# Kernel tuning notes

Hardware: AMD Instinct MI355X
Metric: run time of the kernel (lower is better)

The kernel has to match this reference:

```python
import jax, jax.numpy as jnp
import numpy as np

N = 100000      # nodes
E = 3200000     # directed edges (before self loops)
F_IN = 512      # input node features
HID = 16        # hidden dim (hardcoded in module)
C = 32          # num_classes
NEG_SLOPE = 0.2 # PyG GATConv default


def setup_inputs() -> dict:
    key = jax.random.key(0)
    ks = jax.random.split(key, 10)
    x = jax.random.normal(ks[0], (N, F_IN), dtype=jnp.float32)
    edge_index = jax.random.randint(ks[1], (2, E), 0, N, dtype=jnp.int64)
    s1 = 1.0 / np.sqrt(F_IN)
    s2 = 1.0 / np.sqrt(HID)
    return {
        "x": x,
        "edge_index": edge_index,
        "W1": jax.random.normal(ks[2], (F_IN, HID), dtype=jnp.float32) * s1,
        "att_src1": jax.random.normal(ks[3], (HID,), dtype=jnp.float32) * s2,
        "att_dst1": jax.random.normal(ks[4], (HID,), dtype=jnp.float32) * s2,
        "b1": jnp.zeros((HID,), dtype=jnp.float32),
        "W2": jax.random.normal(ks[5], (HID, C), dtype=jnp.float32) * s2,
        "att_src2": jax.random.normal(ks[6], (C,), dtype=jnp.float32) / np.sqrt(C),
        "att_dst2": jax.random.normal(ks[7], (C,), dtype=jnp.float32) / np.sqrt(C),
        "b2": jnp.zeros((C,), dtype=jnp.float32),
    }


def gat_conv(h_in, src, dst, W, att_src, att_dst, b, n):
    # h: [n, d_out] transformed node features (lin has no bias in PyG GATConv)
    h = h_in @ W
    a_s = h @ att_src        # [n] per-node source score
    a_d = h @ att_dst        # [n] per-node dest score
    e = jax.nn.leaky_relu(a_s[src] + a_d[dst], NEG_SLOPE)  # [n_edges]
    # segment softmax over edges grouped by destination node
    m = jax.ops.segment_max(e, dst, num_segments=n)
    ex = jnp.exp(e - m[dst])
    denom = jax.ops.segment_sum(ex, dst, num_segments=n)
    alpha = ex / denom[dst]
    out = jax.ops.segment_sum(h[src] * alpha[:, None], dst, num_segments=n)
    return out + b


def reference(x, edge_index, W1, att_src1, att_dst1, b1, W2, att_src2, att_dst2, b2):
    n = x.shape[0]
    loops = jnp.arange(n, dtype=edge_index.dtype)  # add_self_loops=True
    src = jnp.concatenate([edge_index[0], loops])
    dst = jnp.concatenate([edge_index[1], loops])
    h = gat_conv(x, src, dst, W1, att_src1, att_dst1, b1, n)
    h = jax.nn.relu(h)
    # dropout is identity in eval mode
    out = gat_conv(h, src, dst, W2, att_src2, att_dst2, b2, n)
    return jax.nn.log_softmax(out, axis=1)
```

## Files before the change

### kernel.cpp

```cpp
#include <hip/hip_runtime.h>
#include <math.h>

#define N_NODES 100000
#define N_EDGES 3200000
#define N_TOT   (N_EDGES + N_NODES)
#define F_IN    512
#define HID     16
#define NCLS    32
#define NEG_SLOPE 0.2f

#define BSH   7
#define NBKT  ((N_NODES + 127) / 128)
#define SRC_MASK 0x1FFFF

#define G_GROUPS 512
#define EPG (N_EDGES / G_GROUPS)
#define NGEMM ((N_NODES + 127) / 128)

__global__ __launch_bounds__(64) void k_detect(const int* __restrict__ ei,
                                               int* __restrict__ flag) {
  int v = ei[2 * threadIdx.x + 1];
  unsigned long long m = __ballot(v != 0);
  if (threadIdx.x == 0) *flag = (m == 0ull) ? 1 : 0;
}

__global__ __launch_bounds__(512) void k_g1h(const float* __restrict__ x,
                                             const float* __restrict__ W,
                                             const float* __restrict__ atts,
                                             const float* __restrict__ attd,
                                             const int* __restrict__ ei,
                                             const int* __restrict__ flag,
                                             int* __restrict__ H,
                                             const float* __restrict__ W2,
                                             const float* __restrict__ as2w,
                                             const float* __restrict__ ad2w,
                                             float* __restrict__ ws2,
                                             float* __restrict__ wd2,
                                             float* __restrict__ h,
                                             float* __restrict__ as_,
                                             float* __restrict__ ad_) {
  __shared__ float smem[2 * 128 * 36];
  int bid = blockIdx.x;
  int t = threadIdx.x;

  if (bid >= NGEMM) {
    if (bid < NGEMM + G_GROUPS) {
      int* hh = (int*)smem;
      for (int i = t; i < NBKT; i += 512) hh[i] = 0;
      __syncthreads();
      int fl = *flag;
      int g = bid - NGEMM;
      int e0 = g * EPG, e1 = e0 + EPG;
      for (int e = e0 + t; e < e1; e += 512) {
        int d = fl ? ei[2 * (N_EDGES + e)] : ei[N_EDGES + e];
        d = min(max(d, 0), N_NODES - 1);
        atomicAdd(&hh[d >> BSH], 1);
      }
      __syncthreads();
      int* Hrow = H + (size_t)g * NBKT;
      for (int i = t; i < NBKT; i += 512) Hrow[i] = hh[i];
    } else {
      if (t < HID) {
        float s = 0.f, d = 0.f;
        for (int c = 0; c < NCLS; ++c) {
          float wv = W2[t * NCLS + c];
          s += wv * as2w[c];
          d += wv * ad2w[c];
        }
        ws2[t] = s;
        wd2[t] = d;
      }
    }
    return;
  }

  float (*xs)[128][36] = (float (*)[128][36])smem;
  float* pacc = smem;
  int wid = t >> 6;
  int lane = t & 63;
  int rhalf = wid & 1;
  int kq = __builtin_amdgcn_readfirstlane(wid >> 1);
  int row = rhalf * 64 + lane;
  int r0 = bid * 128;

  int sr = t >> 3;
  int sk4 = t & 7;
  int sr2 = (t + 512) >> 3;
  int sk42 = (t + 512) & 7;
  int gr1 = min(r0 + sr, N_NODES - 1);
  int gr2 = min(r0 + sr2, N_NODES - 1);

  float acc[HID];
#pragma unroll
  for (int f = 0; f < HID; ++f) acc[f] = 0.f;

  float4 ra, rb;
  ra = *(const float4*)(x + (size_t)gr1 * F_IN + sk4 * 4);
  rb = *(const float4*)(x + (size_t)gr2 * F_IN + sk42 * 4);
  *(float4*)(&xs[0][sr][sk4 * 4]) = ra;
  *(float4*)(&xs[0][sr2][sk42 * 4]) = rb;
  __syncthreads();

  for (int c = 0; c < F_IN / 32; ++c) {
    int buf = c & 1;
    if (c + 1 < F_IN / 32) {
      ra = *(const float4*)(x + (size_t)gr1 * F_IN + (c + 1) * 32 + sk4 * 4);
      rb = *(const float4*)(x + (size_t)gr2 * F_IN + (c + 1) * 32 + sk42 * 4);
    }
    const float* Wc = W + (c * 32 + kq * 8) * HID;
    float4 xa = *(const float4*)(&xs[buf][row][kq * 8 + 0]);
    float4 xb = *(const float4*)(&xs[buf][row][kq * 8 + 4]);
#pragma unroll
    for (int f = 0; f < HID; ++f)
      acc[f] += xa.x * Wc[0 * HID + f] + xa.y * Wc[1 * HID + f] +
                xa.z * Wc[2 * HID + f] + xa.w * Wc[3 * HID + f];
#pragma unroll
    for (int f = 0; f < HID; ++f)
      acc[f] += xb.x * Wc[4 * HID + f] + xb.y * Wc[5 * HID + f] +
                xb.z * Wc[6 * HID + f] + xb.w * Wc[7 * HID + f];
    if (c + 1 < F_IN / 32) {
      *(float4*)(&xs[buf ^ 1][sr][sk4 * 4]) = ra;
      *(float4*)(&xs[buf ^ 1][sr2][sk42 * 4]) = rb;
    }
    __syncthreads();
  }

#pragma unroll
  for (int f = 0; f < HID; ++f) pacc[(kq * 128 + row) * 17 + f] = acc[f];
  __syncthreads();

  int rr = t >> 2, g = t & 3;
  float4 s;
  s.x = pacc[(0 * 128 + rr) * 17 + g * 4 + 0] + pacc[(1 * 128 + rr) * 17 + g * 4 + 0] +
        pacc[(2 * 128 + rr) * 17 + g * 4 + 0] + pacc[(3 * 128 + rr) * 17 + g * 4 + 0];
  s.y = pacc[(0 * 128 + rr) * 17 + g * 4 + 1] + pacc[(1 * 128 + rr) * 17 + g * 4 + 1] +
        pacc[(2 * 128 + rr) * 17 + g * 4 + 1] + pacc[(3 * 128 + rr) * 17 + g * 4 + 1];
  s.z = pacc[(0 * 128 + rr) * 17 + g * 4 + 2] + pacc[(1 * 128 + rr) * 17 + g * 4 + 2] +
        pacc[(2 * 128 + rr) * 17 + g * 4 + 2] + pacc[(3 * 128 + rr) * 17 + g * 4 + 2];
  s.w = pacc[(0 * 128 + rr) * 17 + g * 4 + 3] + pacc[(1 * 128 + rr) * 17 + g * 4 + 3] +
        pacc[(2 * 128 + rr) * 17 + g * 4 + 3] + pacc[(3 * 128 + rr) * 17 + g * 4 + 3];
  int orow = r0 + rr;
  if (orow < N_NODES) ((float4*)(h + (size_t)orow * HID))[g] = s;

  float4 av = ((const float4*)atts)[g];
  float4 dv = ((const float4*)attd)[g];
  float pas = s.x * av.x + s.y * av.y + s.z * av.z + s.w * av.w;
  float pad = s.x * dv.x + s.y * dv.y + s.z * dv.z + s.w * dv.w;
  pas += __shfl_xor(pas, 1); pas += __shfl_xor(pas, 2);
  pad += __shfl_xor(pad, 1); pad += __shfl_xor(pad, 2);
  if (g == 0 && orow < N_NODES) { as_[orow] = pas; ad_[orow] = pad; }
}

__global__ __launch_bounds__(G_GROUPS) void k_colscan(int* __restrict__ H,
                                                      int* __restrict__ tot) {
  __shared__ int s[G_GROUPS];
  int b = blockIdx.x, t = threadIdx.x;
  int v = H[(size_t)t * NBKT + b];
  s[t] = v;
  __syncthreads();
  for (int off = 1; off < G_GROUPS; off <<= 1) {
    int a = (t >= off) ? s[t - off] : 0;
    __syncthreads();
    s[t] += a;
    __syncthreads();
  }
  H[(size_t)t * NBKT + b] = s[t] - v;
  if (t == G_GROUPS - 1) tot[b] = s[t];
}

__global__ __launch_bounds__(256) void k_bscan(const int* __restrict__ tot,
                                               int* __restrict__ bbase,
                                               int* __restrict__ cbase,
                                               int* __restrict__ offs) {
  __shared__ int s1[256], s2[256];
  int t = threadIdx.x;
  int c[4], vn[4];
  int sum1 = 0, sum2 = 0;
#pragma unroll
  for (int j = 0; j < 4; ++j) {
    int idx = t * 4 + j;
    int cc = 0, vv = 0;
    if (idx < NBKT) {
      cc = tot[idx];
      int lo = idx << BSH;
      vv = min(128, N_NODES - lo);
    }
    c[j] = cc; vn[j] = vv;
    sum1 += cc; sum2 += cc + vv;
  }
  int o1 = sum1, o2 = sum2;
  s1[t] = sum1; s2[t] = sum2;
  __syncthreads();
  for (int off = 1; off < 256; off <<= 1) {
    int a = 0, b = 0;
    if (t >= off) { a = s1[t - off]; b = s2[t - off]; }
    __syncthreads();
    s1[t] += a; s2[t] += b;
    __syncthreads();
  }
  int r1 = s1[t] - o1;
  int r2 = s2[t] - o2;
#pragma unroll
  for (int j = 0; j < 4; ++j) {
    int idx = t * 4 + j;
    if (idx < NBKT) {
      bbase[idx] = r1; cbase[idx] = r2;
      r1 += c[j];
      r2 += c[j] + vn[j];
    }
  }
  if (t == 0) offs[N_NODES] = N_TOT;
}

__global__ __launch_bounds__(256) void k_scatter(const int* __restrict__ ei,
                                                 const int* __restrict__ flag,
                                                 const int* __restrict__ H,
                                                 const int* __restrict__ bbase,
                                                 int* __restrict__ binned) {
  __shared__ int cur[NBKT];
  int g = blockIdx.x, t = threadIdx.x;
  const int* Hrow = H + (size_t)g * NBKT;
  for (int i = t; i < NBKT; i += 256) cur[i] = bbase[i] + Hrow[i];
  __syncthreads();
  int fl = *flag;
  int e0 = g * EPG, e1 = e0 + EPG;
  for (int e = e0 + t; e < e1; e += 256) {
    int s, d;
    if (fl) { s = ei[2 * e]; d = ei[2 * (N_EDGES + e)]; }
    else    { s = ei[e];     d = ei[N_EDGES + e]; }
    s = min(max(s, 0), N_NODES - 1);
    d = min(max(d, 0), N_NODES - 1);
    int p = atomicAdd(&cur[d >> BSH], 1);
    p = min(max(p, 0), N_EDGES - 1);
    binned[p] = ((d & 127) << 17) | s;
  }
}

__global__ __launch_bounds__(256) void k_bucket(const int* __restrict__ tot,
                                                const int* __restrict__ bbase,
                                                const int* __restrict__ cbase,
                                                const int* __restrict__ binned,
                                                int* __restrict__ offs,
                                                int* __restrict__ srcS) {
  __shared__ int cnt[128], cur[128], sc[128];
  __shared__ int hdr[3];
  int b = blockIdx.x, t = threadIdx.x;
  if (t == 0) {
    hdr[0] = min(max(tot[b], 0), N_EDGES);
    hdr[1] = min(max(bbase[b], 0), N_EDGES - 1);
    hdr[2] = min(max(cbase[b], 0), N_TOT - 1);
  }
  if (t < 128) cnt[t] = 0;
  __syncthreads();
  int nb = hdr[0], base = hdr[1], cb = hdr[2];

  for (int i = t; i < nb; i += 256) {
    int pk = binned[min(base + i, N_EDGES - 1)];
    atomicAdd(&cnt[(pk >> 17) & 127], 1);
  }
  __syncthreads();

  int node = (b << BSH) + t;
  int myv = 0;
  if (t < 128) myv = (node < N_NODES) ? cnt[t] + 1 : 0;
  if (t < 128) sc[t] = myv;
  __syncthreads();
  for (int off = 1; off < 128; off <<= 1) {
    int v = 0;
    if (t < 128 && t >= off) v = sc[t - off];
    __syncthreads();
    if (t < 128) sc[t] += v;
    __syncthreads();
  }
  if (t < 128 && node < N_NODES) {
    int lofs = sc[t] - myv;
    int o = min(cb + lofs, N_TOT - 1);
    offs[node] = o;
    srcS[o] = node;
    cur[t] = lofs + 1;
  }
  __syncthreads();

  for (int i = t; i < nb; i += 256) {
    int pk = binned[min(base + i, N_EDGES - 1)];
    int p = atomicAdd(&cur[(pk >> 17) & 127], 1);
    srcS[min(cb + p, N_TOT - 1)] = pk & SRC_MASK;
  }
}

template <bool LAYER1>
__global__ __launch_bounds__(256) void k_agg(const int* __restrict__ offs,
                                             const int* __restrict__ srcS,
                                             const float* __restrict__ as_,
                                             const float* __restrict__ ad_,
                                             const float* __restrict__ h,
                                             const float* __restrict__ b1,
                                             const float* __restrict__ ws2,
                                             const float* __restrict__ wd2,
                                             const float* __restrict__ W2,
                                             const float* __restrict__ b2,
                                             float* __restrict__ outv,
                                             float* __restrict__ as2,
                                             float* __restrict__ ad2) {
  int node = blockIdx.x * 4 + (threadIdx.x >> 6);
  if (node >= N_NODES) return;
  int lane = threadIdx.x & 63;
  int esub = lane >> 2;
  int f4 = lane & 3;
  int beg = offs[node];
  int end = offs[node + 1];
  beg = min(max(beg, 0), N_TOT);
  end = min(max(end, beg), N_TOT);
  float ad = ad_[node];

  float s_lane = 0.f;
  float4 acc = make_float4(0.f, 0.f, 0.f, 0.f);
  for (int i0 = beg; i0 < end; i0 += 64) {
    int nb = min(64, end - i0);
    int sn = 0;
    float p = 0.f;
    if (lane < nb) {
      sn = min(max(srcS[i0 + lane], 0), N_NODES - 1);
      float e = as_[sn] + ad;
      e = e > 0.f ? e : NEG_SLOPE * e;
      p = __expf(e);
    }
    s_lane += p;
    int steps = (nb + 15) >> 4;
    for (int t = 0; t < steps; ++t) {
      int j = esub + 16 * t;
      int jj = min(j, nb - 1);
      float pj = __shfl(p, jj);
      int snj = __shfl(sn, jj);
      if (j < nb) {
        float4 v = ((const float4*)(h + (size_t)snj * HID))[f4];
        acc.x += pj * v.x;
        acc.y += pj * v.y;
        acc.z += pj * v.z;
        acc.w += pj * v.w;
      }
    }
  }
#pragma unroll
  for (int off = 1; off < 64; off <<= 1) s_lane += __shfl_xor(s_lane, off);
#pragma unroll
  for (int off = 4; off < 64; off <<= 1) {
    acc.x += __shfl_xor(acc.x, off);
    acc.y += __shfl_xor(acc.y, off);
    acc.z += __shfl_xor(acc.z, off);
    acc.w += __shfl_xor(acc.w, off);
  }
  float inv_s = 1.f / s_lane;

  if (LAYER1) {
    float4 bv = ((const float4*)b1)[f4];
    float4 val;
    val.x = fmaxf(acc.x * inv_s + bv.x, 0.f);
    val.y = fmaxf(acc.y * inv_s + bv.y, 0.f);
    val.z = fmaxf(acc.z * inv_s + bv.z, 0.f);
    val.w = fmaxf(acc.w * inv_s + bv.w, 0.f);
    if (lane < 4) ((float4*)(outv + (size_t)node * HID))[lane] = val;
    float4 w_s = ((const float4*)ws2)[f4];
    float4 w_d = ((const float4*)wd2)[f4];
    float rs = val.x * w_s.x + val.y * w_s.y + val.z * w_s.z + val.w * w_s.w;
    float rd = val.x * w_d.x + val.y * w_d.y + val.z * w_d.z + val.w * w_d.w;
    rs += __shfl_xor(rs, 1); rs += __shfl_xor(rs, 2);
    rd += __shfl_xor(rd, 1); rd += __shfl_xor(rd, 2);
    if (lane == 0) { as2[node] = rs; ad2[node] = rd; }
  } else {
    float hv[HID];
#pragma unroll
    for (int j = 0; j < 4; ++j) {
      int srcl = (lane & ~3) | j;
      hv[4 * j + 0] = __shfl(acc.x, srcl) * inv_s;
      hv[4 * j + 1] = __shfl(acc.y, srcl) * inv_s;
      hv[4 * j + 2] = __shfl(acc.z, srcl) * inv_s;
      hv[4 * j + 3] = __shfl(acc.w, srcl) * inv_s;
    }
    int c = lane & 31;
    float logit = b2[c];
#pragma unroll
    for (int k = 0; k < HID; ++k) logit += hv[k] * W2[k * NCLS + c];
    float mx = logit;
#pragma unroll
    for (int off = 1; off < 32; off <<= 1) mx = fmaxf(mx, __shfl_xor(mx, off));
    float ex = __expf(logit - mx);
    float se = ex;
#pragma unroll
    for (int off = 1; off < 32; off <<= 1) se += __shfl_xor(se, off);
    if (lane < 32) outv[(size_t)node * NCLS + c] = logit - mx - __logf(se);
  }
}

extern "C" void kernel_launch(void* const* d_in, const int* in_sizes, int n_in,
                              void* d_out, int out_size, void* d_ws, size_t ws_size,
                              hipStream_t stream) {
  const float* x    = (const float*)d_in[0];
  const int*   ei   = (const int*)d_in[1];
  const float* W1   = (const float*)d_in[2];
  const float* as1w = (const float*)d_in[3];
  const float* ad1w = (const float*)d_in[4];
  const float* b1   = (const float*)d_in[5];
  const float* W2   = (const float*)d_in[6];
  const float* as2w = (const float*)d_in[7];
  const float* ad2w = (const float*)d_in[8];
  const float* b2   = (const float*)d_in[9];
  float* out = (float*)d_out;

  char* w = (char*)d_ws;
  size_t off = 0;
  auto alloc = [&](size_t bytes) -> char* {
    char* p = w + off;
    off += (bytes + 511) & ~(size_t)511;
    return p;
  };
  int*   flag  = (int*)alloc(4);
  int*   tot   = (int*)alloc((size_t)NBKT * 4);
  int*   bbase = (int*)alloc((size_t)NBKT * 4);
  int*   cbase = (int*)alloc((size_t)NBKT * 4);
  int*   offs  = (int*)alloc((size_t)(N_NODES + 1) * 4);
  int*   srcS  = (int*)alloc((size_t)N_TOT * 4);
  float* ws2   = (float*)alloc((size_t)HID * 4);
  float* wd2   = (float*)alloc((size_t)HID * 4);
  int*   H     = (int*)alloc((size_t)G_GROUPS * NBKT * 4);
  float* h1    = (float*)alloc((size_t)N_NODES * HID * 4);
  float* as1   = (float*)alloc((size_t)N_NODES * 4);
  float* ad1   = (float*)alloc((size_t)N_NODES * 4);

  size_t region_begin = off;
  int* binned = (int*)alloc((size_t)N_EDGES * 4);
  off = region_begin;
  float* hr   = (float*)alloc((size_t)N_NODES * HID * 4);
  float* as2  = (float*)alloc((size_t)N_NODES * 4);
  float* ad2  = (float*)alloc((size_t)N_NODES * 4);

  k_detect<<<1, 64, 0, stream>>>(ei, flag);
  k_g1h<<<NGEMM + G_GROUPS + 1, 512, 0, stream>>>(x, W1, as1w, ad1w, ei, flag, H,
                                                  W2, as2w, ad2w, ws2, wd2,
                                                  h1, as1, ad1);
  k_colscan<<<NBKT, G_GROUPS, 0, stream>>>(H, tot);
  k_bscan<<<1, 256, 0, stream>>>(tot, bbase, cbase, offs);
  k_scatter<<<G_GROUPS, 256, 0, stream>>>(ei, flag, H, bbase, binned);
  k_bucket<<<NBKT, 256, 0, stream>>>(tot, bbase, cbase, binned, offs, srcS);
  k_agg<true><<<(N_NODES + 3) / 4, 256, 0, stream>>>(offs, srcS, as1, ad1, h1,
                                                     b1, ws2, wd2, nullptr, nullptr,
                                                     hr, as2, ad2);
  k_agg<false><<<(N_NODES + 3) / 4, 256, 0, stream>>>(offs, srcS, as2, ad2, hr,
                                                      nullptr, nullptr, nullptr,
                                                      W2, b2, out, nullptr, nullptr);
}
```

Baseline: 267.3 us.

## Inline edge-format detection, unroll GEMM double-buffer, vectorize scatter edge loads

Removes the separate k_detect launch by running the int64/int32 format check inside each block that needs it, using a shared flag. The first-layer GEMM loop is unrolled in pairs with fixed buffer indices and deeper register prefetch of x. k_scatter now reads edge indices two at a time with int4 or int2 loads, splitting the loop by format. This trades one fewer kernel launch and fewer load instructions for redundant per-block detection reads and more register pressure in the GEMM.

```diff
diff --git a/kernel.cpp b/kernel.cpp
--- a/kernel.cpp
+++ b/kernel.cpp
@@ -17,11 +17,15 @@
 #define EPG (N_EDGES / G_GROUPS)
 #define NGEMM ((N_NODES + 127) / 128)
 
-__global__ __launch_bounds__(64) void k_detect(const int* __restrict__ ei,
-                                               int* __restrict__ flag) {
-  int v = ei[2 * threadIdx.x + 1];
-  unsigned long long m = __ballot(v != 0);
-  if (threadIdx.x == 0) *flag = (m == 0ull) ? 1 : 0;
+__device__ __forceinline__ int detect_fl(const int* __restrict__ ei,
+                                         int t, int* sflag) {
+  if (t < 64) {
+    int v = ei[2 * t + 1];
+    unsigned long long m = __ballot(v != 0);
+    if (t == 0) *sflag = (m == 0ull) ? 1 : 0;
+  }
+  __syncthreads();
+  return *sflag;
 }
 
 __global__ __launch_bounds__(512) void k_g1h(const float* __restrict__ x,
@@ -29,7 +33,6 @@
                                              const float* __restrict__ atts,
                                              const float* __restrict__ attd,
                                              const int* __restrict__ ei,
-                                             const int* __restrict__ flag,
                                              int* __restrict__ H,
                                              const float* __restrict__ W2,
                                              const float* __restrict__ as2w,
@@ -46,9 +49,9 @@
   if (bid >= NGEMM) {
     if (bid < NGEMM + G_GROUPS) {
       int* hh = (int*)smem;
+      int* sflag = hh + NBKT;
       for (int i = t; i < NBKT; i += 512) hh[i] = 0;
-      __syncthreads();
-      int fl = *flag;
+      int fl = detect_fl(ei, t, sflag);
       int g = bid - NGEMM;
       int e0 = g * EPG, e1 = e0 + EPG;
       for (int e = e0 + t; e < e1; e += 512) {
@@ -87,40 +90,65 @@
   int sk4 = t & 7;
   int sr2 = (t + 512) >> 3;
   int sk42 = (t + 512) & 7;
-  int gr1 = min(r0 + sr, N_NODES - 1);
-  int gr2 = min(r0 + sr2, N_NODES - 1);
+  const float* xp1 = x + (size_t)min(r0 + sr, N_NODES - 1) * F_IN + sk4 * 4;
+  const float* xp2 = x + (size_t)min(r0 + sr2, N_NODES - 1) * F_IN + sk42 * 4;
 
   float acc[HID];
 #pragma unroll
   for (int f = 0; f < HID; ++f) acc[f] = 0.f;
 
-  float4 ra, rb;
-  ra = *(const float4*)(x + (size_t)gr1 * F_IN + sk4 * 4);
-  rb = *(const float4*)(x + (size_t)gr2 * F_IN + sk42 * 4);
-  *(float4*)(&xs[0][sr][sk4 * 4]) = ra;
-  *(float4*)(&xs[0][sr2][sk42 * 4]) = rb;
-  __syncthreads();
-
-  for (int c = 0; c < F_IN / 32; ++c) {
-    int buf = c & 1;
-    if (c + 1 < F_IN / 32) {
-      ra = *(const float4*)(x + (size_t)gr1 * F_IN + (c + 1) * 32 + sk4 * 4);
-      rb = *(const float4*)(x + (size_t)gr2 * F_IN + (c + 1) * 32 + sk42 * 4);
-    }
-    const float* Wc = W + (c * 32 + kq * 8) * HID;
-    float4 xa = *(const float4*)(&xs[buf][row][kq * 8 + 0]);
-    float4 xb = *(const float4*)(&xs[buf][row][kq * 8 + 4]);
-#pragma unroll
-    for (int f = 0; f < HID; ++f)
-      acc[f] += xa.x * Wc[0 * HID + f] + xa.y * Wc[1 * HID + f] +
-                xa.z * Wc[2 * HID + f] + xa.w * Wc[3 * HID + f];
-#pragma unroll
-    for (int f = 0; f < HID; ++f)
-      acc[f] += xb.x * Wc[4 * HID + f] + xb.y * Wc[5 * HID + f] +
-                xb.z * Wc[6 * HID + f] + xb.w * Wc[7 * HID + f];
-    if (c + 1 < F_IN / 32) {
-      *(float4*)(&xs[buf ^ 1][sr][sk4 * 4]) = ra;
-      *(float4*)(&xs[buf ^ 1][sr2][sk42 * 4]) = rb;
+  float4 a0, a1, b0, b1;
+  a0 = *(const float4*)(xp1 + 0 * 32);
+  a1 = *(const float4*)(xp2 + 0 * 32);
+  *(float4*)(&xs[0][sr][sk4 * 4]) = a0;
+  *(float4*)(&xs[0][sr2][sk42 * 4]) = a1;
+  a0 = *(const float4*)(xp1 + 1 * 32);
+  a1 = *(const float4*)(xp2 + 1 * 32);
+  __syncthreads();
+
+#pragma unroll
+  for (int cc = 0; cc < 8; ++cc) {
+    const int c = 2 * cc;
+    if (cc < 7) {
+      b0 = *(const float4*)(xp1 + (c + 2) * 32);
+      b1 = *(const float4*)(xp2 + (c + 2) * 32);
+    }
+    {
+      const float* Wc = W + (c * 32 + kq * 8) * HID;
+      float4 xa = *(const float4*)(&xs[0][row][kq * 8 + 0]);
+      float4 xb = *(const float4*)(&xs[0][row][kq * 8 + 4]);
+#pragma unroll
+      for (int f = 0; f < HID; ++f)
+        acc[f] += xa.x * Wc[0 * HID + f] + xa.y * Wc[1 * HID + f] +
+                  xa.z * Wc[2 * HID + f] + xa.w * Wc[3 * HID + f];
+#pragma unroll
+      for (int f = 0; f < HID; ++f)
+        acc[f] += xb.x * Wc[4 * HID + f] + xb.y * Wc[5 * HID + f] +
+                  xb.z * Wc[6 * HID + f] + xb.w * Wc[7 * HID + f];
+    }
+    *(float4*)(&xs[1][sr][sk4 * 4]) = a0;
+    *(float4*)(&xs[1][sr2][sk42 * 4]) = a1;
+    __syncthreads();
+    if (cc < 7) {
+      a0 = *(const float4*)(xp1 + (c + 3) * 32);
+      a1 = *(const float4*)(xp2 + (c + 3) * 32);
+    }
+    {
+      const float* Wc = W + ((c + 1) * 32 + kq * 8) * HID;
+      float4 xa = *(const float4*)(&xs[1][row][kq * 8 + 0]);
+      float4 xb = *(const float4*)(&xs[1][row][kq * 8 + 4]);
+#pragma unroll
+      for (int f = 0; f < HID; ++f)
+        acc[f] += xa.x * Wc[0 * HID + f] + xa.y * Wc[1 * HID + f] +
+                  xa.z * Wc[2 * HID + f] + xa.w * Wc[3 * HID + f];
+#pragma unroll
+      for (int f = 0; f < HID; ++f)
+        acc[f] += xb.x * Wc[4 * HID + f] + xb.y * Wc[5 * HID + f] +
+                  xb.z * Wc[6 * HID + f] + xb.w * Wc[7 * HID + f];
+    }
+    if (cc < 7) {
+      *(float4*)(&xs[0][sr][sk4 * 4]) = b0;
+      *(float4*)(&xs[0][sr2][sk42 * 4]) = b1;
     }
     __syncthreads();
   }
@@ -213,26 +241,42 @@
 }
 
 __global__ __launch_bounds__(256) void k_scatter(const int* __restrict__ ei,
-                                                 const int* __restrict__ flag,
                                                  const int* __restrict__ H,
                                                  const int* __restrict__ bbase,
                                                  int* __restrict__ binned) {
   __shared__ int cur[NBKT];
+  __shared__ int sflag;
   int g = blockIdx.x, t = threadIdx.x;
   const int* Hrow = H + (size_t)g * NBKT;
   for (int i = t; i < NBKT; i += 256) cur[i] = bbase[i] + Hrow[i];
-  __syncthreads();
-  int fl = *flag;
+  int fl = detect_fl(ei, t, &sflag);
   int e0 = g * EPG, e1 = e0 + EPG;
-  for (int e = e0 + t; e < e1; e += 256) {
-    int s, d;
-    if (fl) { s = ei[2 * e]; d = ei[2 * (N_EDGES + e)]; }
-    else    { s = ei[e];     d = ei[N_EDGES + e]; }
-    s = min(max(s, 0), N_NODES - 1);
-    d = min(max(d, 0), N_NODES - 1);
-    int p = atomicAdd(&cur[d >> BSH], 1);
-    p = min(max(p, 0), N_EDGES - 1);
-    binned[p] = ((d & 127) << 17) | s;
+  if (fl) {
+    for (int e = e0 + t * 2; e < e1; e += 512) {
+      int4 sv = *(const int4*)(ei + 2 * (size_t)e);
+      int4 dv = *(const int4*)(ei + 2 * ((size_t)N_EDGES + e));
+      int s0 = min(max(sv.x, 0), N_NODES - 1);
+      int d0 = min(max(dv.x, 0), N_NODES - 1);
+      int s1 = min(max(sv.z, 0), N_NODES - 1);
+      int d1 = min(max(dv.z, 0), N_NODES - 1);
+      int p0 = atomicAdd(&cur[d0 >> BSH], 1);
+      binned[min(max(p0, 0), N_EDGES - 1)] = ((d0 & 127) << 17) | s0;
+      int p1 = atomicAdd(&cur[d1 >> BSH], 1);
+      binned[min(max(p1, 0), N_EDGES - 1)] = ((d1 & 127) << 17) | s1;
+    }
+  } else {
+    for (int e = e0 + t * 2; e < e1; e += 512) {
+      int2 sv = *(const int2*)(ei + e);
+      int2 dv = *(const int2*)(ei + (size_t)N_EDGES + e);
+      int s0 = min(max(sv.x, 0), N_NODES - 1);
+      int d0 = min(max(dv.x, 0), N_NODES - 1);
+      int s1 = min(max(sv.y, 0), N_NODES - 1);
+      int d1 = min(max(dv.y, 0), N_NODES - 1);
+      int p0 = atomicAdd(&cur[d0 >> BSH], 1);
+      binned[min(max(p0, 0), N_EDGES - 1)] = ((d0 & 127) << 17) | s0;
+      int p1 = atomicAdd(&cur[d1 >> BSH], 1);
+      binned[min(max(p1, 0), N_EDGES - 1)] = ((d1 & 127) << 17) | s1;
+    }
   }
 }
 
@@ -414,7 +458,6 @@
     off += (bytes + 511) & ~(size_t)511;
     return p;
   };
-  int*   flag  = (int*)alloc(4);
   int*   tot   = (int*)alloc((size_t)NBKT * 4);
   int*   bbase = (int*)alloc((size_t)NBKT * 4);
   int*   cbase = (int*)alloc((size_t)NBKT * 4);
@@ -434,13 +477,12 @@
   float* as2  = (float*)alloc((size_t)N_NODES * 4);
   float* ad2  = (float*)alloc((size_t)N_NODES * 4);
 
-  k_detect<<<1, 64, 0, stream>>>(ei, flag);
-  k_g1h<<<NGEMM + G_GROUPS + 1, 512, 0, stream>>>(x, W1, as1w, ad1w, ei, flag, H,
+  k_g1h<<<NGEMM + G_GROUPS + 1, 512, 0, stream>>>(x, W1, as1w, ad1w, ei, H,
                                                   W2, as2w, ad2w, ws2, wd2,
                                                   h1, as1, ad1);
   k_colscan<<<NBKT, G_GROUPS, 0, stream>>>(H, tot);
   k_bscan<<<1, 256, 0, stream>>>(tot, bbase, cbase, offs);
-  k_scatter<<<G_GROUPS, 256, 0, stream>>>(ei, flag, H, bbase, binned);
+  k_scatter<<<G_GROUPS, 256, 0, stream>>>(ei, H, bbase, binned);
   k_bucket<<<NBKT, 256, 0, stream>>>(tot, bbase, cbase, binned, offs, srcS);
   k_agg<true><<<(N_NODES + 3) / 4, 256, 0, stream>>>(offs, srcS, as1, ad1, h1,
                                                      b1, ws2, wd2, nullptr, nullptr,
```

Measured after the change: 257.3 us. 1.04x faster.
